# Performance work log

Hardware: AMD Instinct MI355X
Metric: run time of the kernel (lower is better)

## Reference

```python
import jax, jax.numpy as jnp
import numpy as np

N_NODES = 16
N_EDGES = 64
N_LAYERS = 4


def _gcn(x, src, dst, emask, W, b):
    # PyG GCNConv: add self-loops, symmetric deg^-1/2 normalization, sum-aggregate.
    n = x.shape[0]
    h = x @ W  # [n, d_out]
    deg = jax.ops.segment_sum(emask, dst, num_segments=n) + 1.0  # +1 self-loop
    dinv = jax.lax.rsqrt(deg)
    norm = dinv[src] * dinv[dst] * emask  # masked-out edges get 0 weight
    out = jax.ops.segment_sum(norm[:, None] * h[src], dst, num_segments=n)
    return out + (dinv * dinv)[:, None] * h + b  # self-loop term + bias


def _sag_pool(x, src, dst, emask, w_rel, b_rel, w_root, k):
    # SAGPooling with GraphConv scorer: score = lin_rel(sum_j x_j) + lin_root(x)
    n = x.shape[0]
    agg = jax.ops.segment_sum(emask[:, None] * x[src], dst, num_segments=n)
    score = agg @ w_rel + b_rel + x @ w_root  # [n]
    perm = jnp.argsort(-score)[:k]  # top-k nodes
    x_new = x[perm] * jnp.tanh(score[perm])[:, None]
    kept = jnp.zeros(n, bool).at[perm].set(True)
    pos = jnp.zeros(n, jnp.int32).at[perm].set(jnp.arange(k, dtype=jnp.int32))
    emask_new = emask * kept[src] * kept[dst]  # drop edges touching removed nodes
    return x_new, pos[src], pos[dst], emask_new


def _conv_gnn(x, src, dst, W0, Ws, bs, pWrel, pbrel, pWroot, linW, linb):
    emask = jnp.ones(src.shape[0], x.dtype)
    n = x.shape[0]
    for i in range(N_LAYERS):
        W = W0 if i == 0 else Ws[i - 1]
        x = jax.nn.relu(_gcn(x, src, dst, emask, W, bs[i]))
        k = -(-n // 2)  # ceil(0.5 * n) -- SAGPooling ratio=0.5
        x, src, dst, emask = _sag_pool(x, src, dst, emask, pWrel[i], pbrel[i], pWroot[i], k)
        n = k
    x = x @ linW + linb  # [1, 128]
    return jax.nn.log_softmax(x, axis=1)


def _fc(h, fcW, fcb, lnw, lnb):
    eps = 1e-5
    for i in range(3):
        h = h @ fcW[i] + fcb[i]
        mu = h.mean(-1, keepdims=True)
        var = ((h - mu) ** 2).mean(-1, keepdims=True)
        h = (h - mu) * jax.lax.rsqrt(var + eps) * lnw[i] + lnb[i]
        h = jax.nn.relu(h)
    return h @ fcW[3] + fcb[3]


def setup_inputs() -> dict:
    key = jax.random.key(0)
    ks = iter(jax.random.split(key, 64))

    def rn(shape, s=0.05):
        return jax.random.normal(next(ks), shape, jnp.float32) * s

    def gnn_params(p):
        return {
            p + '_W0': rn((45, 128)), p + '_W': rn((3, 128, 128)),
            p + '_b': jnp.zeros((4, 128), jnp.float32),
            p + '_pWrel': rn((4, 128)), p + '_pbrel': jnp.zeros((4,), jnp.float32),
            p + '_pWroot': rn((4, 128)),
            p + '_linW': rn((128, 128)), p + '_linb': jnp.zeros((128,), jnp.float32),
        }

    inp = {
        'gp_x': rn((N_NODES, 45), 1.0), 'sp_x': rn((N_NODES, 45), 1.0),
        'gp_src': jax.random.randint(next(ks), (N_EDGES,), 0, N_NODES, jnp.int32),
        'gp_dst': jax.random.randint(next(ks), (N_EDGES,), 0, N_NODES, jnp.int32),
        'sp_src': jax.random.randint(next(ks), (N_EDGES,), 0, N_NODES, jnp.int32),
        'sp_dst': jax.random.randint(next(ks), (N_EDGES,), 0, N_NODES, jnp.int32),
        'fcW': rn((4, 256, 256)), 'fcb': jnp.zeros((4, 256), jnp.float32),
        'lnw': jnp.ones((3, 256), jnp.float32), 'lnb': jnp.zeros((3, 256), jnp.float32),
    }
    inp.update(gnn_params('g'))
    inp.update(gnn_params('s'))
    return inp


def reference(gp_x, sp_x, gp_src, gp_dst, sp_src, sp_dst,
              g_W0, g_W, g_b, g_pWrel, g_pbrel, g_pWroot, g_linW, g_linb,
              s_W0, s_W, s_b, s_pWrel, s_pbrel, s_pWroot, s_linW, s_linb,
              fcW, fcb, lnw, lnb):
    out1 = _conv_gnn(gp_x, gp_src, gp_dst, g_W0, g_W, g_b, g_pWrel, g_pbrel, g_pWroot, g_linW, g_linb)
    out2 = _conv_gnn(sp_x, sp_src, sp_dst, s_W0, s_W, s_b, s_pWrel, s_pbrel, s_pWroot, s_linW, s_linb)
    concat = jnp.concatenate((out1.reshape(-1), out2.reshape(-1)))  # [256]
    return _fc(concat, fcW, fcb, lnw, lnb)
```

## Files before the change

kernel.cpp:

```cpp
#include <hip/hip_runtime.h>
#include <math.h>

#define MAGIC 0x5F3759DFu
typedef unsigned int u32;

__device__ __forceinline__ void bar_lds(){
  asm volatile("s_waitcnt lgkmcnt(0)\n\ts_barrier" ::: "memory");
}
__device__ __forceinline__ void bar_full(){
  asm volatile("s_waitcnt vmcnt(0) lgkmcnt(0)\n\ts_barrier" ::: "memory");
}

__device__ inline float wsum(float v){
  #pragma unroll
  for (int o=32;o;o>>=1) v += __shfl_xor(v,o,64);
  return v;
}
__device__ inline float wmax(float v){
  #pragma unroll
  for (int o=32;o;o>>=1) v = fmaxf(v,__shfl_xor(v,o,64));
  return v;
}

__device__ __forceinline__ void stageW(const float* g, float* l, int nfloats,
                                       int wid, int lane){
  const int nch = nfloats>>8;
  for (int c=wid; c<nch; c+=8)
    __builtin_amdgcn_global_load_lds(
      (__attribute__((address_space(1))) u32*)(void*)(g+(c<<8)+(lane<<2)),
      (__attribute__((address_space(3))) u32*)(void*)(l+(c<<8)), 16, 0, 0);
}

__device__ __forceinline__ void pf(const float* p, int nfloats, int tid){
  float4 acc={0.f,0.f,0.f,0.f};
  const int nq=nfloats>>2;
  for (int i=tid;i<nq;i+=512){
    const float4 v=((const float4*)p)[i];
    acc.x+=v.x; acc.y+=v.y; acc.z+=v.z; acc.w+=v.w;
  }
  asm volatile("" :: "v"(acc.x),"v"(acc.y),"v"(acc.z),"v"(acc.w));
}

__global__ __launch_bounds__(512,1) void net_kernel(
    const float* __restrict__ gp_x, const float* __restrict__ sp_x,
    const int* __restrict__ gp_src, const int* __restrict__ gp_dst,
    const int* __restrict__ sp_src, const int* __restrict__ sp_dst,
    const float* __restrict__ g_W0, const float* __restrict__ g_W,
    const float* __restrict__ g_b,  const float* __restrict__ g_pWrel,
    const float* __restrict__ g_pbrel, const float* __restrict__ g_pWroot,
    const float* __restrict__ g_linW, const float* __restrict__ g_linb,
    const float* __restrict__ s_W0, const float* __restrict__ s_W,
    const float* __restrict__ s_b,  const float* __restrict__ s_pWrel,
    const float* __restrict__ s_pbrel, const float* __restrict__ s_pWroot,
    const float* __restrict__ s_linW, const float* __restrict__ s_linb,
    const float* __restrict__ fcW, const float* __restrict__ fcb,
    const float* __restrict__ lnw, const float* __restrict__ lnb,
    float* __restrict__ wsbuf, float* __restrict__ out)
{
  __shared__ float slotA[16384];
  __shared__ float slotB[16384];
  __shared__ float XBx[16][132];
  __shared__ float ZB[16][132];
  __shared__ float PBf[2048];
  __shared__ float wrelL[512], wrootL[512];
  __shared__ float fcin[256], yA[128];
  __shared__ float wpart[16];
  __shared__ int   esrcA[64]; __shared__ float ewA[64];
  __shared__ int   cntA[16], startA[16];
  __shared__ float dinvA[16], tsA[8];
  __shared__ int   permA[8];

  const int lt  = threadIdx.x;
  const int bid = blockIdx.x;
  const int wid = lt>>6, lane = lt&63;

  if (bid >= 6){
    switch(bid){
      case 8:  pf(g_W0,5760,lt);        pf(g_W,32768,lt);      break;
      case 9:  pf(s_W0,5760,lt);        pf(s_W,32768,lt);      break;
      case 6:  pf(g_W+32768,16384,lt);  pf(g_linW,16384,lt);
               pf(g_pWrel,512,lt);      pf(g_pWroot,512,lt);   break;
      case 7:  pf(s_W+32768,16384,lt);  pf(s_linW,16384,lt);
               pf(s_pWrel,512,lt);      pf(s_pWroot,512,lt);   break;
      case 10: pf(fcW,65536,lt);        break;
      case 11: pf(fcW+65536,65536,lt);  break;
      case 12: pf(fcW+131072,65536,lt); break;
      case 13: pf(fcW+196608,65536,lt); break;
      case 14: pf(fcb,1024,lt); pf(lnw,768,lt); pf(lnb,768,lt); break;
      default: break;
    }
    return;
  }

  if (bid >= 2){
    const int L = bid-2;
    const int qfc=(wid<<3)+(lane&7), f0fc=(lane>>3)<<5;
    float4 wr[32];
    #pragma unroll
    for (int t=0;t<32;++t) wr[t]=*(const float4*)(fcW+(L<<16)+(f0fc+t)*256+(qfc<<2));
    const float4 bb=*(const float4*)(fcb+(L<<8)+(qfc<<2));
    float4 lw={0,0,0,0}, lb2={0,0,0,0};
    if (L<3){ lw=*(const float4*)(lnw+(L<<8)+(qfc<<2)); lb2=*(const float4*)(lnb+(L<<8)+(qfc<<2)); }
    if (lt==0){
      if (L==0){
        const u32* f1=(const u32*)(wsbuf+128);
        const u32* f2=(const u32*)(wsbuf+384);
        while (__hip_atomic_load(f1,__ATOMIC_ACQUIRE,__HIP_MEMORY_SCOPE_AGENT)!=MAGIC ||
               __hip_atomic_load(f2,__ATOMIC_ACQUIRE,__HIP_MEMORY_SCOPE_AGENT)!=MAGIC)
          __builtin_amdgcn_s_sleep(1);
      } else {
        const u32* f1=(const u32*)(wsbuf+512+(L-1)*512+256);
        while (__hip_atomic_load(f1,__ATOMIC_ACQUIRE,__HIP_MEMORY_SCOPE_AGENT)!=MAGIC)
          __builtin_amdgcn_s_sleep(1);
      }
    }
    bar_lds();
    if (lt<256){
      const float* src = (L==0) ? (wsbuf + (lt<128 ? lt : 128+lt))
                                : (wsbuf + 512 + (L-1)*512 + lt);
      fcin[lt]=__hip_atomic_load(src,__ATOMIC_RELAXED,__HIP_MEMORY_SCOPE_AGENT);
    }
    bar_lds();
    float4 a={0.f,0.f,0.f,0.f};
    #pragma unroll
    for (int t=0;t<32;++t){
      const float zv=fcin[f0fc+t];
      a.x+=zv*wr[t].x; a.y+=zv*wr[t].y; a.z+=zv*wr[t].z; a.w+=zv*wr[t].w;
    }
    #pragma unroll
    for (int m=8;m<64;m<<=1){
      a.x+=__shfl_xor(a.x,m,64); a.y+=__shfl_xor(a.y,m,64);
      a.z+=__shfl_xor(a.z,m,64); a.w+=__shfl_xor(a.w,m,64);
    }
    if (L==3){
      if (lane<8){
        float4 r; r.x=a.x+bb.x; r.y=a.y+bb.y; r.z=a.z+bb.z; r.w=a.w+bb.w;
        *(float4*)(out+(qfc<<2))=r;
      }
      return;
    }
    const bool act=(lane<8);
    float4 hv={0.f,0.f,0.f,0.f};
    if (act){
      hv.x=a.x+bb.x; hv.y=a.y+bb.y; hv.z=a.z+bb.z; hv.w=a.w+bb.w;
      float s=hv.x+hv.y+hv.z+hv.w;
      float s2=hv.x*hv.x+hv.y*hv.y+hv.z*hv.z+hv.w*hv.w;
      #pragma unroll
      for (int m=1;m<8;m<<=1){ s+=__shfl_xor(s,m,64); s2+=__shfl_xor(s2,m,64); }
      if (lane==0){ wpart[wid]=s; wpart[8+wid]=s2; }
    }
    bar_lds();
    if (act){
      float S=0.f,S2=0.f;
      #pragma unroll
      for (int w2=0;w2<8;++w2){ S+=wpart[w2]; S2+=wpart[8+w2]; }
      const float mu=S*(1.f/256.f);
      const float ri=rsqrtf(S2*(1.f/256.f)-mu*mu+1e-5f);
      float* dst=wsbuf+512+L*512+(qfc<<2);
      __hip_atomic_store(dst+0, fmaxf((hv.x-mu)*ri*lw.x+lb2.x,0.f), __ATOMIC_RELAXED,__HIP_MEMORY_SCOPE_AGENT);
      __hip_atomic_store(dst+1, fmaxf((hv.y-mu)*ri*lw.y+lb2.y,0.f), __ATOMIC_RELAXED,__HIP_MEMORY_SCOPE_AGENT);
      __hip_atomic_store(dst+2, fmaxf((hv.z-mu)*ri*lw.z+lb2.z,0.f), __ATOMIC_RELAXED,__HIP_MEMORY_SCOPE_AGENT);
      __hip_atomic_store(dst+3, fmaxf((hv.w-mu)*ri*lw.w+lb2.w,0.f), __ATOMIC_RELAXED,__HIP_MEMORY_SCOPE_AGENT);
    }
    __threadfence();
    bar_lds();
    if (lt==0) __hip_atomic_store((u32*)(wsbuf+512+L*512+256), MAGIC, __ATOMIC_RELEASE,__HIP_MEMORY_SCOPE_AGENT);
    return;
  }

  const int br = bid;
  const float* x0    = br ? sp_x    : gp_x;
  const int*   srcg  = br ? sp_src  : gp_src;
  const int*   dstg  = br ? sp_dst  : gp_dst;
  const float* W0    = br ? s_W0    : g_W0;
  const float* Wl    = br ? s_W     : g_W;
  const float* bl    = br ? s_b     : g_b;
  const float* wrel  = br ? s_pWrel : g_pWrel;
  const float* brel  = br ? s_pbrel : g_pbrel;
  const float* wroot = br ? s_pWroot: g_pWroot;
  const float* linW  = br ? s_linW  : g_linW;
  const float* linb  = br ? s_linb  : g_linb;
  float* wsOut = wsbuf + br*256;
  u32*   wsFlag = (u32*)(wsbuf + 128 + br*256);

  float xv[4];
  #pragma unroll
  for (int r=0;r<4;++r){
    const int i=lt+(r<<9), v=i>>7, f=i&127;
    xv[r] = (f<45)? x0[v*45+f] : 0.f;
  }
  int es=0, ed=0; float emk=0.f;
  if (lt<64){ es=srcg[lt]; ed=dstg[lt]; emk=1.f; }
  const float4 brelv = *(const float4*)brel;
  asm volatile("" ::: "memory");

  stageW(Wl,        slotA, 16384, wid, lane);
  stageW(Wl+16384,  slotB, 16384, wid, lane);
  stageW(wrel,  wrelL,  512, wid, lane);
  stageW(wroot, wrootL, 512, wid, lane);

  auto build_csr = [&](int n, float tsrc){
    unsigned long long mymask=0ull; int mystart=0, run=0, mycnt=0, mystartnode=0;
    const bool act = (emk!=0.f);
    for (int v=0; v<n; ++v){
      const unsigned long long m = __ballot(act && (ed==v));
      const int pc = __popcll(m);
      if (ed==v){ mymask=m; mystart=run; }
      if (lt==v){ mycnt=pc; mystartnode=run; }
      run += pc;
    }
    const float dinvlane = rsqrtf(1.f+(float)mycnt);
    const float dvs = __shfl(dinvlane, es, 64);
    const float dvd = __shfl(dinvlane, ed, 64);
    if (act){
      const int idx = mystart + __popcll(mymask & ((1ull<<lt)-1ull));
      esrcA[idx]=es; ewA[idx]=dvs*dvd*tsrc;
    }
    if (lt<n){ cntA[lt]=mycnt; startA[lt]=mystartnode; dinvA[lt]=dinvlane; }
  };

  #pragma unroll
  for (int r=0;r<4;++r){
    const int i=lt+(r<<9), v=i>>7, f=i&127;
    XBx[v][f]=xv[r];
  }
  if (lt<64) build_csr(16, 1.f);
  bar_lds();

  #pragma unroll
  for (int layer=0; layer<4; ++layer){
    const int n=16>>layer, k=n>>1;

    if (layer==0){
      if (lt<256){
        const int v=lt>>4, j4=(lt&15)<<2;
        if (j4<48){
          const float dv=dinvA[v], dv2=dv*dv;
          float4 a=*(const float4*)&XBx[v][j4];
          a.x*=dv2; a.y*=dv2; a.z*=dv2; a.w*=dv2;
          const int st=startA[v], cn=cntA[v];
          for (int i=0;i<cn;++i){
            const int s=esrcA[st+i]; const float w=ewA[st+i];
            const float4 xs=*(const float4*)&XBx[s][j4];
            a.x+=w*xs.x; a.y+=w*xs.y; a.z+=w*xs.z; a.w+=w*xs.w;
          }
          *(float4*)&ZB[v][j4]=a;
        }
      }
    } else {
      if (lt < (n<<5)){
        const int v=lt>>5, j4=(lt&31)<<2;
        const int pv=permA[v];
        const float dv=dinvA[v];
        const float sw=dv*dv*tsA[v];
        float4 a=*(const float4*)&XBx[pv][j4];
        a.x*=sw; a.y*=sw; a.z*=sw; a.w*=sw;
        const int st=startA[v], cn=cntA[v];
        for (int i=0;i<cn;++i){
          const int srow=permA[esrcA[st+i]]; const float w=ewA[st+i];
          const float4 xs=*(const float4*)&XBx[srow][j4];
          a.x+=w*xs.x; a.y+=w*xs.y; a.z+=w*xs.z; a.w+=w*xs.w;
        }
        *(float4*)&ZB[v][j4]=a;
      }
    }
    if (layer==3) bar_full();
    else          bar_lds();

    if (layer==0){
      const int v=lt>>5, j4=(lt&31)<<2;
      const float* zrow=&ZB[v][0];
      const float4 b4=*(const float4*)(bl+j4);
      float4 a={0.f,0.f,0.f,0.f};
      #pragma unroll
      for (int bb=0;bb<2;++bb){
        float4 wr[16]; float zr[16];
        #pragma unroll
        for (int t=0;t<16;++t){ wr[t]=*(const float4*)(W0+(bb*16+t)*128+j4); zr[t]=zrow[bb*16+t]; }
        #pragma unroll
        for (int t=0;t<16;++t){ a.x+=zr[t]*wr[t].x; a.y+=zr[t]*wr[t].y; a.z+=zr[t]*wr[t].z; a.w+=zr[t]*wr[t].w; }
      }
      { float4 wr[13]; float zr[13];
        #pragma unroll
        for (int t=0;t<13;++t){ wr[t]=*(const float4*)(W0+(32+t)*128+j4); zr[t]=zrow[32+t]; }
        #pragma unroll
        for (int t=0;t<13;++t){ a.x+=zr[t]*wr[t].x; a.y+=zr[t]*wr[t].y; a.z+=zr[t]*wr[t].z; a.w+=zr[t]*wr[t].w; }
      }
      XBx[v][j4+0]=fmaxf(a.x+b4.x,0.f);
      XBx[v][j4+1]=fmaxf(a.y+b4.y,0.f);
      XBx[v][j4+2]=fmaxf(a.z+b4.z,0.f);
      XBx[v][j4+3]=fmaxf(a.w+b4.w,0.f);
      bar_full();
    } else {
      const float* slot=(layer&1)?slotA:slotB;
      const int sh=9-layer, nq=512>>layer, S=1<<layer, chunk=128>>layer;
      const int q=lt&(nq-1), fh=lt>>sh;
      const int v=q>>5, j4=(q&31)<<2;
      const float* zrow=&ZB[v][0];
      const int f0=fh*chunk;
      float4 a={0.f,0.f,0.f,0.f};
      #pragma unroll
      for (int f=0; f<chunk; ++f){
        const float zv=zrow[f0+f];
        const float4 w4=*(const float4*)&slot[(f0+f)*128+j4];
        a.x+=zv*w4.x; a.y+=zv*w4.y; a.z+=zv*w4.z; a.w+=zv*w4.w;
      }
      *(float4*)&PBf[lt<<2]=a;
      bar_lds();
      if (lt<nq){
        float4 acc=*(const float4*)(bl+layer*128+((lt&31)<<2));
        #pragma unroll
        for (int f2=0; f2<S; ++f2){
          const float4 p=*(const float4*)&PBf[(f2*nq+lt)<<2];
          acc.x+=p.x; acc.y+=p.y; acc.z+=p.z; acc.w+=p.w;
        }
        const int vv=lt>>5, jj4=(lt&31)<<2;
        XBx[vv][jj4+0]=fmaxf(acc.x,0.f);
        XBx[vv][jj4+1]=fmaxf(acc.y,0.f);
        XBx[vv][jj4+2]=fmaxf(acc.z,0.f);
        XBx[vv][jj4+3]=fmaxf(acc.w,0.f);
      }
      bar_lds();
    }

    if (layer==1) stageW(Wl+32768, slotA, 16384, wid, lane);
    if (layer==2) stageW(linW,     slotB, 16384, wid, lane);
    if (lt<64){
      const int lpsh=2+layer, lpn=1<<lpsh, cf4=8>>layer;
      const int v=lt>>lpsh, part=lt&(lpn-1);
      const int f04=part*cf4;
      float p1=0.f,p2=0.f;
      #pragma unroll
      for (int i=0;i<cf4;++i){
        const float4 xw=*(const float4*)&XBx[v][(f04+i)<<2];
        const float4 w4=*(const float4*)&wrelL[layer*128+((f04+i)<<2)];
        const float4 o4=*(const float4*)&wrootL[layer*128+((f04+i)<<2)];
        p1+=xw.x*w4.x+xw.y*w4.y+xw.z*w4.z+xw.w*w4.w;
        p2+=xw.x*o4.x+xw.y*o4.y+xw.z*o4.z+xw.w*o4.w;
      }
      #pragma unroll
      for (int m=1;m<32;m<<=1) if (m<lpn){ p1+=__shfl_xor(p1,m,64); p2+=__shfl_xor(p2,m,64); }
      float sc=-INFINITY;
      if (lt<n){
        const float bv = (layer==0)?brelv.x:(layer==1)?brelv.y:(layer==2)?brelv.z:brelv.w;
        sc=__shfl(p2, lt<<lpsh, 64) + bv;
        const int st=startA[lt], cn=cntA[lt];
        for (int i=0;i<cn;++i) sc += __shfl(p1, esrcA[st+i]<<lpsh, 64);
      }
      int rank=0;
      for (int u=0;u<n;++u){
        const float su=__shfl(sc,u,64);
        rank += (su>sc || (su==sc && u<lt)) ? 1:0;
      }
      const int kept=(lt<n && rank<k)?1:0;
      const int pos=kept?rank:0;
      const float tval = kept? tanhf(sc) : 0.f;
      if (kept){ permA[rank]=lt; tsA[rank]=tval; }
      const float ts_src = __shfl(tval, es, 64);
      const int ks=__shfl(kept,es,64), kd=__shfl(kept,ed,64);
      const int ps=__shfl(pos,es,64),  pd=__shfl(pos,ed,64);
      emk *= (float)(ks&kd);
      es=ps; ed=pd;
      if (layer<3) build_csr(k, ts_src);
    }
    bar_lds();
  }

  {
    const int oj=(wid<<4)+(lane>>2);
    const int f0=(lane&3)<<5;
    const int prow=permA[0]; const float tsf=tsA[0];
    const float lb=linb[oj];
    float p=0.f;
    #pragma unroll
    for (int f=0; f<32; ++f) p += XBx[prow][f0+f]*slotB[(f0+f)*128+oj];
    p += __shfl_xor(p,1,64); p += __shfl_xor(p,2,64);
    if ((lane&3)==0) yA[oj]=p*tsf+lb;
  }
  bar_lds();
  if (lt<128){
    const int ln=lt&63;
    const float a0=yA[ln], b0=yA[64+ln];
    const float m=wmax(fmaxf(a0,b0));
    const float sum=wsum(expf(a0-m)+expf(b0-m));
    const float lse=m+logf(sum);
    __hip_atomic_store(&wsOut[lt], yA[lt]-lse, __ATOMIC_RELAXED, __HIP_MEMORY_SCOPE_AGENT);
  }
  __threadfence();
  bar_lds();
  if (lt==0) __hip_atomic_store(wsFlag, MAGIC, __ATOMIC_RELEASE, __HIP_MEMORY_SCOPE_AGENT);
}

extern "C" void kernel_launch(void* const* d_in, const int* in_sizes, int n_in,
                              void* d_out, int out_size, void* d_ws, size_t ws_size,
                              hipStream_t stream){
  net_kernel<<<16,512,0,stream>>>(
    (const float*)d_in[0],(const float*)d_in[1],
    (const int*)d_in[2],(const int*)d_in[3],(const int*)d_in[4],(const int*)d_in[5],
    (const float*)d_in[10],(const float*)d_in[11],(const float*)d_in[12],(const float*)d_in[13],
    (const float*)d_in[14],(const float*)d_in[15],(const float*)d_in[16],(const float*)d_in[17],
    (const float*)d_in[18],(const float*)d_in[19],(const float*)d_in[20],(const float*)d_in[21],
    (const float*)d_in[22],(const float*)d_in[23],(const float*)d_in[24],(const float*)d_in[25],
    (const float*)d_in[6],(const float*)d_in[7],(const float*)d_in[8],(const float*)d_in[9],
    (float*)d_ws,(float*)d_out);
}
```

Before: 26.48 us.

## Replace CSR aggregation with dense adjacency and fuse GCN matmul with pool scoring

Replaces the per-layer CSR build with a small dense 16x16 normalized adjacency matrix (built with LDS atomics) and a count matrix for the SAGPool aggregation. Each layer's GCN matmul now reduces its split-K partials with cross-lane shuffles and immediately computes the pool score dot products, removing the separate partial buffer pass and its barriers. Weight staging is re-sequenced, and partial vmcnt waits let later global-to-LDS loads stay in flight during compute. The dense loops do O(n^2) work and the atomics add contention, but the graphs are tiny.

```diff
diff --git a/kernel.cpp b/kernel.cpp
--- a/kernel.cpp
+++ b/kernel.cpp
@@ -7,8 +7,11 @@
 __device__ __forceinline__ void bar_lds(){
   asm volatile("s_waitcnt lgkmcnt(0)\n\ts_barrier" ::: "memory");
 }
-__device__ __forceinline__ void bar_full(){
+__device__ __forceinline__ void bar_vm0(){
   asm volatile("s_waitcnt vmcnt(0) lgkmcnt(0)\n\ts_barrier" ::: "memory");
+}
+__device__ __forceinline__ void bar_vm8(){
+  asm volatile("s_waitcnt vmcnt(8) lgkmcnt(0)\n\ts_barrier" ::: "memory");
 }
 
 __device__ inline float wsum(float v){
@@ -21,7 +24,11 @@
   for (int o=32;o;o>>=1) v = fmaxf(v,__shfl_xor(v,o,64));
   return v;
 }
-
+__device__ inline float hsum32(float v){
+  #pragma unroll
+  for (int o=16;o;o>>=1) v += __shfl_xor(v,o,64);
+  return v;
+}
 __device__ __forceinline__ void stageW(const float* g, float* l, int nfloats,
                                        int wid, int lane){
   const int nch = nfloats>>8;
@@ -30,7 +37,6 @@
       (__attribute__((address_space(1))) u32*)(void*)(g+(c<<8)+(lane<<2)),
       (__attribute__((address_space(3))) u32*)(void*)(l+(c<<8)), 16, 0, 0);
 }
-
 __device__ __forceinline__ void pf(const float* p, int nfloats, int tid){
   float4 acc={0.f,0.f,0.f,0.f};
   const int nq=nfloats>>2;
@@ -39,6 +45,45 @@
     acc.x+=v.x; acc.y+=v.y; acc.z+=v.z; acc.w+=v.w;
   }
   asm volatile("" :: "v"(acc.x),"v"(acc.y),"v"(acc.z),"v"(acc.w));
+}
+
+template<int L>
+__device__ __forceinline__ void cfused(int lt, const float* slot, const float* ZBp,
+    float (*XB)[128], const float* wrelL, const float* wrootL,
+    float4 blv, float* d1P, float* d2P){
+  const int SPL=1<<L, CH=128>>L;
+  const int o=lt>>L, part=lt&(SPL-1);
+  const int v=o>>5, c4=o&31, f0=part*CH;
+  const float* zrow = ZBp + v*128;
+  float4 a={0.f,0.f,0.f,0.f};
+  #pragma unroll
+  for (int f=0; f<CH; ++f){
+    const float zv=zrow[f0+f];
+    const float4 w4=*(const float4*)&slot[(f0+f)*128+(c4<<2)];
+    a.x+=zv*w4.x; a.y+=zv*w4.y; a.z+=zv*w4.z; a.w+=zv*w4.w;
+  }
+  #pragma unroll
+  for (int m=1;m<SPL;m<<=1){
+    a.x+=__shfl_xor(a.x,m,64); a.y+=__shfl_xor(a.y,m,64);
+    a.z+=__shfl_xor(a.z,m,64); a.w+=__shfl_xor(a.w,m,64);
+  }
+  float p1=0.f,p2=0.f;
+  if (part==0){
+    float4 ox;
+    ox.x=fmaxf(a.x+blv.x,0.f); ox.y=fmaxf(a.y+blv.y,0.f);
+    ox.z=fmaxf(a.z+blv.z,0.f); ox.w=fmaxf(a.w+blv.w,0.f);
+    *(float4*)&XB[v][c4<<2]=ox;
+    const float4 wr4=*(const float4*)&wrelL[(L<<7)+(c4<<2)];
+    const float4 wo4=*(const float4*)&wrootL[(L<<7)+(c4<<2)];
+    p1=ox.x*wr4.x+ox.y*wr4.y+ox.z*wr4.z+ox.w*wr4.w;
+    p2=ox.x*wo4.x+ox.y*wo4.y+ox.z*wo4.z+ox.w*wo4.w;
+  }
+  p1=wsum(p1); p2=wsum(p2);
+  const int wid=lt>>6, lane=lt&63;
+  if (lane==0){
+    const int vv=wid>>(L-1), wp=wid&((1<<(L-1))-1);
+    d1P[(vv<<2)+wp]=p1; d2P[(vv<<2)+wp]=p2;
+  }
 }
 
 __global__ __launch_bounds__(512,1) void net_kernel(
@@ -57,18 +102,16 @@
     const float* __restrict__ lnw, const float* __restrict__ lnb,
     float* __restrict__ wsbuf, float* __restrict__ out)
 {
-  __shared__ float slotA[16384];
-  __shared__ float slotB[16384];
-  __shared__ float XBx[16][132];
-  __shared__ float ZB[16][132];
-  __shared__ float PBf[2048];
-  __shared__ float wrelL[512], wrootL[512];
-  __shared__ float fcin[256], yA[128];
-  __shared__ float wpart[16];
-  __shared__ int   esrcA[64]; __shared__ float ewA[64];
-  __shared__ int   cntA[16], startA[16];
-  __shared__ float dinvA[16], tsA[8];
-  __shared__ int   permA[8];
+  __shared__ __align__(16) float slotA[16384];
+  __shared__ __align__(16) float slotB[16384];
+  __shared__ __align__(16) float XBx[16][128];
+  __shared__ __align__(16) float ZBraw[1024];
+  __shared__ __align__(16) float wrelL[512], wrootL[512];
+  __shared__ __align__(16) float Adn[256], Mdn[256];
+  __shared__ float d1P[64], d2P[64];
+  __shared__ float yA[128];
+  __shared__ float tsA[8]; __shared__ int permA[8];
+  __shared__ float fcin[256]; __shared__ float wpart[16];
 
   const int lt  = threadIdx.x;
   const int bid = blockIdx.x;
@@ -157,14 +200,14 @@
       const float mu=S*(1.f/256.f);
       const float ri=rsqrtf(S2*(1.f/256.f)-mu*mu+1e-5f);
       float* dst=wsbuf+512+L*512+(qfc<<2);
-      __hip_atomic_store(dst+0, fmaxf((hv.x-mu)*ri*lw.x+lb2.x,0.f), __ATOMIC_RELAXED,__HIP_MEMORY_SCOPE_AGENT);
-      __hip_atomic_store(dst+1, fmaxf((hv.y-mu)*ri*lw.y+lb2.y,0.f), __ATOMIC_RELAXED,__HIP_MEMORY_SCOPE_AGENT);
-      __hip_atomic_store(dst+2, fmaxf((hv.z-mu)*ri*lw.z+lb2.z,0.f), __ATOMIC_RELAXED,__HIP_MEMORY_SCOPE_AGENT);
-      __hip_atomic_store(dst+3, fmaxf((hv.w-mu)*ri*lw.w+lb2.w,0.f), __ATOMIC_RELAXED,__HIP_MEMORY_SCOPE_AGENT);
+      __hip_atomic_store(dst+0,fmaxf((hv.x-mu)*ri*lw.x+lb2.x,0.f),__ATOMIC_RELAXED,__HIP_MEMORY_SCOPE_AGENT);
+      __hip_atomic_store(dst+1,fmaxf((hv.y-mu)*ri*lw.y+lb2.y,0.f),__ATOMIC_RELAXED,__HIP_MEMORY_SCOPE_AGENT);
+      __hip_atomic_store(dst+2,fmaxf((hv.z-mu)*ri*lw.z+lb2.z,0.f),__ATOMIC_RELAXED,__HIP_MEMORY_SCOPE_AGENT);
+      __hip_atomic_store(dst+3,fmaxf((hv.w-mu)*ri*lw.w+lb2.w,0.f),__ATOMIC_RELAXED,__HIP_MEMORY_SCOPE_AGENT);
     }
     __threadfence();
     bar_lds();
-    if (lt==0) __hip_atomic_store((u32*)(wsbuf+512+L*512+256), MAGIC, __ATOMIC_RELEASE,__HIP_MEMORY_SCOPE_AGENT);
+    if (lt==0) __hip_atomic_store((u32*)(wsbuf+512+L*512+256),MAGIC,__ATOMIC_RELEASE,__HIP_MEMORY_SCOPE_AGENT);
     return;
   }
 
@@ -178,7 +221,7 @@
   const float* wrel  = br ? s_pWrel : g_pWrel;
   const float* brel  = br ? s_pbrel : g_pbrel;
   const float* wroot = br ? s_pWroot: g_pWroot;
-  const float* linW  = br ? s_linW  : g_linW;
+  const float* linWg = br ? s_linW  : g_linW;
   const float* linb  = br ? s_linb  : g_linb;
   float* wsOut = wsbuf + br*256;
   u32*   wsFlag = (u32*)(wsbuf + 128 + br*256);
@@ -192,160 +235,49 @@
   int es=0, ed=0; float emk=0.f;
   if (lt<64){ es=srcg[lt]; ed=dstg[lt]; emk=1.f; }
   const float4 brelv = *(const float4*)brel;
+  const float4 blv0=*(const float4*)(bl       + ((lt&31)<<2));
+  const float4 blv1=*(const float4*)(bl + 128 + (((lt>>1)&31)<<2));
+  const float4 blv2=*(const float4*)(bl + 256 + (((lt>>2)&31)<<2));
+  const float4 blv3=*(const float4*)(bl + 384 + (((lt>>3)&31)<<2));
+  const float linb_s = linb[lt>>2];
   asm volatile("" ::: "memory");
-
-  stageW(Wl,        slotA, 16384, wid, lane);
-  stageW(Wl+16384,  slotB, 16384, wid, lane);
   stageW(wrel,  wrelL,  512, wid, lane);
   stageW(wroot, wrootL, 512, wid, lane);
-
-  auto build_csr = [&](int n, float tsrc){
-    unsigned long long mymask=0ull; int mystart=0, run=0, mycnt=0, mystartnode=0;
-    const bool act = (emk!=0.f);
-    for (int v=0; v<n; ++v){
-      const unsigned long long m = __ballot(act && (ed==v));
-      const int pc = __popcll(m);
-      if (ed==v){ mymask=m; mystart=run; }
-      if (lt==v){ mycnt=pc; mystartnode=run; }
-      run += pc;
-    }
-    const float dinvlane = rsqrtf(1.f+(float)mycnt);
-    const float dvs = __shfl(dinvlane, es, 64);
-    const float dvd = __shfl(dinvlane, ed, 64);
+  stageW(Wl,    slotA, 16384, wid, lane);
+
+  auto build_dense=[&](int kk, float wlane, bool with_ts){
+    const float4 z4={0.f,0.f,0.f,0.f};
+    *(float4*)&Adn[lt<<2]=z4;
+    *(float4*)&Mdn[lt<<2]=z4;
+    const bool act=(emk!=0.f);
+    int mycnt=0;
+    for (int v=0;v<kk;++v){
+      const unsigned long long m=__ballot(act&&(ed==v));
+      if (lt==v) mycnt=__popcll(m);
+    }
+    const float dinvl=rsqrtf(1.f+(float)mycnt);
+    const float dvs=__shfl(dinvl,es,64);
+    const float dvd=__shfl(dinvl,ed,64);
     if (act){
-      const int idx = mystart + __popcll(mymask & ((1ull<<lt)-1ull));
-      esrcA[idx]=es; ewA[idx]=dvs*dvd*tsrc;
-    }
-    if (lt<n){ cntA[lt]=mycnt; startA[lt]=mystartnode; dinvA[lt]=dinvlane; }
+      atomicAdd(&Adn[ed*16+es], dvs*dvd*wlane);
+      atomicAdd(&Mdn[ed*16+es], 1.f);
+    }
+    if (lt<kk){
+      const float tv = with_ts ? tsA[lt] : 1.f;
+      atomicAdd(&Adn[lt*17], dinvl*dinvl*tv);
+    }
   };
-
-  #pragma unroll
-  for (int r=0;r<4;++r){
-    const int i=lt+(r<<9), v=i>>7, f=i&127;
-    XBx[v][f]=xv[r];
-  }
-  if (lt<64) build_csr(16, 1.f);
-  bar_lds();
-
-  #pragma unroll
-  for (int layer=0; layer<4; ++layer){
-    const int n=16>>layer, k=n>>1;
-
-    if (layer==0){
-      if (lt<256){
-        const int v=lt>>4, j4=(lt&15)<<2;
-        if (j4<48){
-          const float dv=dinvA[v], dv2=dv*dv;
-          float4 a=*(const float4*)&XBx[v][j4];
-          a.x*=dv2; a.y*=dv2; a.z*=dv2; a.w*=dv2;
-          const int st=startA[v], cn=cntA[v];
-          for (int i=0;i<cn;++i){
-            const int s=esrcA[st+i]; const float w=ewA[st+i];
-            const float4 xs=*(const float4*)&XBx[s][j4];
-            a.x+=w*xs.x; a.y+=w*xs.y; a.z+=w*xs.z; a.w+=w*xs.w;
-          }
-          *(float4*)&ZB[v][j4]=a;
-        }
-      }
-    } else {
-      if (lt < (n<<5)){
-        const int v=lt>>5, j4=(lt&31)<<2;
-        const int pv=permA[v];
-        const float dv=dinvA[v];
-        const float sw=dv*dv*tsA[v];
-        float4 a=*(const float4*)&XBx[pv][j4];
-        a.x*=sw; a.y*=sw; a.z*=sw; a.w*=sw;
-        const int st=startA[v], cn=cntA[v];
-        for (int i=0;i<cn;++i){
-          const int srow=permA[esrcA[st+i]]; const float w=ewA[st+i];
-          const float4 xs=*(const float4*)&XBx[srow][j4];
-          a.x+=w*xs.x; a.y+=w*xs.y; a.z+=w*xs.z; a.w+=w*xs.w;
-        }
-        *(float4*)&ZB[v][j4]=a;
-      }
-    }
-    if (layer==3) bar_full();
-    else          bar_lds();
-
-    if (layer==0){
-      const int v=lt>>5, j4=(lt&31)<<2;
-      const float* zrow=&ZB[v][0];
-      const float4 b4=*(const float4*)(bl+j4);
-      float4 a={0.f,0.f,0.f,0.f};
-      #pragma unroll
-      for (int bb=0;bb<2;++bb){
-        float4 wr[16]; float zr[16];
-        #pragma unroll
-        for (int t=0;t<16;++t){ wr[t]=*(const float4*)(W0+(bb*16+t)*128+j4); zr[t]=zrow[bb*16+t]; }
-        #pragma unroll
-        for (int t=0;t<16;++t){ a.x+=zr[t]*wr[t].x; a.y+=zr[t]*wr[t].y; a.z+=zr[t]*wr[t].z; a.w+=zr[t]*wr[t].w; }
-      }
-      { float4 wr[13]; float zr[13];
-        #pragma unroll
-        for (int t=0;t<13;++t){ wr[t]=*(const float4*)(W0+(32+t)*128+j4); zr[t]=zrow[32+t]; }
-        #pragma unroll
-        for (int t=0;t<13;++t){ a.x+=zr[t]*wr[t].x; a.y+=zr[t]*wr[t].y; a.z+=zr[t]*wr[t].z; a.w+=zr[t]*wr[t].w; }
-      }
-      XBx[v][j4+0]=fmaxf(a.x+b4.x,0.f);
-      XBx[v][j4+1]=fmaxf(a.y+b4.y,0.f);
-      XBx[v][j4+2]=fmaxf(a.z+b4.z,0.f);
-      XBx[v][j4+3]=fmaxf(a.w+b4.w,0.f);
-      bar_full();
-    } else {
-      const float* slot=(layer&1)?slotA:slotB;
-      const int sh=9-layer, nq=512>>layer, S=1<<layer, chunk=128>>layer;
-      const int q=lt&(nq-1), fh=lt>>sh;
-      const int v=q>>5, j4=(q&31)<<2;
-      const float* zrow=&ZB[v][0];
-      const int f0=fh*chunk;
-      float4 a={0.f,0.f,0.f,0.f};
-      #pragma unroll
-      for (int f=0; f<chunk; ++f){
-        const float zv=zrow[f0+f];
-        const float4 w4=*(const float4*)&slot[(f0+f)*128+j4];
-        a.x+=zv*w4.x; a.y+=zv*w4.y; a.z+=zv*w4.z; a.w+=zv*w4.w;
-      }
-      *(float4*)&PBf[lt<<2]=a;
-      bar_lds();
-      if (lt<nq){
-        float4 acc=*(const float4*)(bl+layer*128+((lt&31)<<2));
-        #pragma unroll
-        for (int f2=0; f2<S; ++f2){
-          const float4 p=*(const float4*)&PBf[(f2*nq+lt)<<2];
-          acc.x+=p.x; acc.y+=p.y; acc.z+=p.z; acc.w+=p.w;
-        }
-        const int vv=lt>>5, jj4=(lt&31)<<2;
-        XBx[vv][jj4+0]=fmaxf(acc.x,0.f);
-        XBx[vv][jj4+1]=fmaxf(acc.y,0.f);
-        XBx[vv][jj4+2]=fmaxf(acc.z,0.f);
-        XBx[vv][jj4+3]=fmaxf(acc.w,0.f);
-      }
-      bar_lds();
-    }
-
-    if (layer==1) stageW(Wl+32768, slotA, 16384, wid, lane);
-    if (layer==2) stageW(linW,     slotB, 16384, wid, lane);
+  auto doE=[&](int n,int k,float bv,int nparts,bool rebuild){
     if (lt<64){
-      const int lpsh=2+layer, lpn=1<<lpsh, cf4=8>>layer;
-      const int v=lt>>lpsh, part=lt&(lpn-1);
-      const int f04=part*cf4;
-      float p1=0.f,p2=0.f;
-      #pragma unroll
-      for (int i=0;i<cf4;++i){
-        const float4 xw=*(const float4*)&XBx[v][(f04+i)<<2];
-        const float4 w4=*(const float4*)&wrelL[layer*128+((f04+i)<<2)];
-        const float4 o4=*(const float4*)&wrootL[layer*128+((f04+i)<<2)];
-        p1+=xw.x*w4.x+xw.y*w4.y+xw.z*w4.z+xw.w*w4.w;
-        p2+=xw.x*o4.x+xw.y*o4.y+xw.z*o4.z+xw.w*o4.w;
-      }
-      #pragma unroll
-      for (int m=1;m<32;m<<=1) if (m<lpn){ p1+=__shfl_xor(p1,m,64); p2+=__shfl_xor(p2,m,64); }
+      float d1s=0.f, d2s=0.f;
+      if (lt<n){
+        for (int p=0;p<nparts;++p){ d1s+=d1P[(lt<<2)+p]; d2s+=d2P[(lt<<2)+p]; }
+      }
       float sc=-INFINITY;
       if (lt<n){
-        const float bv = (layer==0)?brelv.x:(layer==1)?brelv.y:(layer==2)?brelv.z:brelv.w;
-        sc=__shfl(p2, lt<<lpsh, 64) + bv;
-        const int st=startA[lt], cn=cntA[lt];
-        for (int i=0;i<cn;++i) sc += __shfl(p1, esrcA[st+i]<<lpsh, 64);
+        float acc=d2s+bv;
+        for (int u=0;u<n;++u) acc += Mdn[lt*16+u]*__shfl(d1s,u,64);
+        sc=acc;
       }
       int rank=0;
       for (int u=0;u<n;++u){
@@ -354,28 +286,113 @@
       }
       const int kept=(lt<n && rank<k)?1:0;
       const int pos=kept?rank:0;
-      const float tval = kept? tanhf(sc) : 0.f;
+      const float tval=kept?tanhf(sc):0.f;
       if (kept){ permA[rank]=lt; tsA[rank]=tval; }
-      const float ts_src = __shfl(tval, es, 64);
+      const float ts_src=__shfl(tval,es,64);
       const int ks=__shfl(kept,es,64), kd=__shfl(kept,ed,64);
       const int ps=__shfl(pos,es,64),  pd=__shfl(pos,ed,64);
       emk *= (float)(ks&kd);
       es=ps; ed=pd;
-      if (layer<3) build_csr(k, ts_src);
-    }
-    bar_lds();
-  }
+      if (rebuild) build_dense(k, ts_src, true);
+    }
+  };
+  auto doB=[&](int n){
+    if (lt<(n<<5)){
+      const int v=lt>>5, j4=(lt&31)<<2;
+      float4 a={0.f,0.f,0.f,0.f};
+      for (int u=0;u<n;++u){
+        const float w=Adn[v*16+u];
+        const float4 xs=*(const float4*)&XBx[permA[u]][j4];
+        a.x+=w*xs.x; a.y+=w*xs.y; a.z+=w*xs.z; a.w+=w*xs.w;
+      }
+      *(float4*)&ZBraw[(v<<7)+j4]=a;
+    }
+  };
+
+  #pragma unroll
+  for (int r=0;r<4;++r){
+    const int i=lt+(r<<9), v=i>>7, f=i&127;
+    XBx[v][f]=xv[r];
+  }
+  if (lt<64) build_dense(16, 1.f, false);
+  bar_lds();
+
+  if (lt<256){
+    const int v=lt>>4, j4=(lt&15)<<2;
+    if (j4<48){
+      float4 a={0.f,0.f,0.f,0.f};
+      for (int u=0;u<16;++u){
+        const float w=Adn[v*16+u];
+        const float4 xs=*(const float4*)&XBx[u][j4];
+        a.x+=w*xs.x; a.y+=w*xs.y; a.z+=w*xs.z; a.w+=w*xs.w;
+      }
+      *(float4*)&ZBraw[v*48+j4]=a;
+    }
+  }
+  bar_vm8();
 
   {
-    const int oj=(wid<<4)+(lane>>2);
-    const int f0=(lane&3)<<5;
-    const int prow=permA[0]; const float tsf=tsA[0];
-    const float lb=linb[oj];
+    const int v=lt>>5, c4=lt&31, j4=c4<<2;
+    const float* zrow=&ZBraw[v*48];
+    float4 a={0.f,0.f,0.f,0.f};
+    #pragma unroll
+    for (int bb=0;bb<2;++bb){
+      float4 wr[16]; float zr[16];
+      #pragma unroll
+      for (int t=0;t<16;++t){ wr[t]=*(const float4*)(W0+(bb*16+t)*128+j4); zr[t]=zrow[bb*16+t]; }
+      #pragma unroll
+      for (int t=0;t<16;++t){ a.x+=zr[t]*wr[t].x; a.y+=zr[t]*wr[t].y; a.z+=zr[t]*wr[t].z; a.w+=zr[t]*wr[t].w; }
+    }
+    { float4 wr[13]; float zr[13];
+      #pragma unroll
+      for (int t=0;t<13;++t){ wr[t]=*(const float4*)(W0+(32+t)*128+j4); zr[t]=zrow[32+t]; }
+      #pragma unroll
+      for (int t=0;t<13;++t){ a.x+=zr[t]*wr[t].x; a.y+=zr[t]*wr[t].y; a.z+=zr[t]*wr[t].z; a.w+=zr[t]*wr[t].w; }
+    }
+    float4 ox;
+    ox.x=fmaxf(a.x+blv0.x,0.f); ox.y=fmaxf(a.y+blv0.y,0.f);
+    ox.z=fmaxf(a.z+blv0.z,0.f); ox.w=fmaxf(a.w+blv0.w,0.f);
+    *(float4*)&XBx[v][j4]=ox;
+    const float4 wr4=*(const float4*)&wrelL[j4];
+    const float4 wo4=*(const float4*)&wrootL[j4];
+    float p1=ox.x*wr4.x+ox.y*wr4.y+ox.z*wr4.z+ox.w*wr4.w;
+    float p2=ox.x*wo4.x+ox.y*wo4.y+ox.z*wo4.z+ox.w*wo4.w;
+    p1=hsum32(p1); p2=hsum32(p2);
+    if ((lane&31)==0){
+      const int vv=(wid<<1)|(lane>>5);
+      d1P[vv<<2]=p1; d2P[vv<<2]=p2;
+    }
+  }
+  stageW(Wl+16384, slotB, 16384, wid, lane);
+  bar_lds();
+
+  doE(16, 8, brelv.x, 1, true);  bar_lds();
+  doB(8);                        bar_vm8();
+  cfused<1>(lt, slotA, ZBraw, XBx, wrelL, wrootL, blv1, d1P, d2P);
+  bar_lds();
+  stageW(Wl+32768, slotA, 16384, wid, lane);
+  doE(8, 4, brelv.y, 1, true);   bar_lds();
+  doB(4);                        bar_vm8();
+  cfused<2>(lt, slotB, ZBraw, XBx, wrelL, wrootL, blv2, d1P, d2P);
+  bar_lds();
+  stageW(linWg, slotB, 16384, wid, lane);
+  doE(4, 2, brelv.z, 2, true);   bar_lds();
+  doB(2);                        bar_vm8();
+  cfused<3>(lt, slotA, ZBraw, XBx, wrelL, wrootL, blv3, d1P, d2P);
+  bar_lds();
+  doE(2, 1, brelv.w, 4, false);  bar_vm0();
+
+  {
+    const int oj=lt>>2, fh=lt&3;
+    const int prow=permA[0];
     float p=0.f;
     #pragma unroll
-    for (int f=0; f<32; ++f) p += XBx[prow][f0+f]*slotB[(f0+f)*128+oj];
-    p += __shfl_xor(p,1,64); p += __shfl_xor(p,2,64);
-    if ((lane&3)==0) yA[oj]=p*tsf+lb;
+    for (int i=0;i<32;++i){
+      const int f=(fh<<5)+i;
+      p += XBx[prow][f]*slotB[f*128+oj];
+    }
+    p+=__shfl_xor(p,1,64); p+=__shfl_xor(p,2,64);
+    if (fh==0) yA[oj]=p*tsA[0]+linb_s;
   }
   bar_lds();
   if (lt<128){
```

New measurement: 27.41 us. 3.5% more time.
